# Optimization experiments

Hardware: AMD Instinct MI355X
Metric: run time of the kernel (lower is better)

Reference implementation:

```python
import jax, jax.numpy as jnp
import numpy as np

N_OBS = 2_097_152
N_BAND = 4
T_SPAN = 3650.0  # days


def setup_inputs() -> dict:
    key = jax.random.key(0)
    k0, k1, k2, k3, k4, k5 = jax.random.split(key, 6)
    t = jnp.sort(jax.random.uniform(k0, (N_OBS,), jnp.float32) * T_SPAN)
    band = jax.random.randint(k1, (N_OBS,), 0, N_BAND)
    y = jax.random.normal(k2, (N_OBS,), jnp.float32)
    yerr = 0.1 + 0.9 * jax.random.uniform(k3, (N_OBS,), jnp.float32)
    log_amp_delta = 0.1 * jax.random.normal(k4, (N_BAND - 1,), jnp.float32)
    # [log sigma, log ell] for the quasisep Exp kernel
    log_kernel_param = jnp.array([0.0, np.log(50.0)], dtype=jnp.float32) + \
        0.1 * jax.random.normal(k5, (2,), jnp.float32)
    return {"t": t, "band": band, "y": y, "yerr": yerr,
            "log_amp_delta": log_amp_delta, "log_kernel_param": log_kernel_param}


def _log_prob(t, band, y, yerr, log_amp_delta, log_kernel_param):
    # amp_transform: prepend 0 -> per-band amplitudes
    amps = jnp.exp(jnp.concatenate([jnp.zeros(1, log_amp_delta.dtype), log_amp_delta]))
    sigma2 = jnp.exp(2.0 * log_kernel_param[0])
    ell = jnp.exp(log_kernel_param[1])

    # lag_transform with zero lags: sort by time (assume_sorted path of tinygp)
    inds = jnp.argsort(t)
    ts, b = t[inds], band[inds]
    ys, dg = y[inds], (yerr ** 2)[inds]

    # multiband Exp kernel: K_ij = sigma2 * u_i * u_j * exp(-(t_i - t_j)/ell), i>=j
    u = amps[b]                       # per-point amplitude
    a = dg + sigma2 * u * u           # diagonal K_ii + noise
    U = sigma2 * u                    # semiseparable left factor
    V = u                             # semiseparable right factor
    dt = jnp.diff(ts)
    P = jnp.concatenate([jnp.zeros(1, ts.dtype), jnp.exp(-dt / ell)])  # decay factors

    # Celerite O(N) Cholesky (K = L D L^T) fused with the forward solve L z = y.
    def step(carry, x):
        cS, cg = carry                # cS = S_{n-1} + D_{n-1} W_{n-1}^2 ; cg = g_{n-1} + W_{n-1} z_{n-1}
        Pn, an, Un, Vn, yn = x
        Sn = Pn * Pn * cS
        gn = Pn * cg
        Dn = an - Un * Un * Sn
        Wn = (Vn - Sn * Un) / Dn
        zn = yn - Un * gn
        return (Sn + Dn * Wn * Wn, gn + Wn * zn), (jnp.log(Dn), zn * zn / Dn)

    zero = jnp.zeros((), ts.dtype)
    _, (logD, quad) = jax.lax.scan(step, (zero, zero), (P, a, U, V, ys))
    n = ts.shape[0]
    return -0.5 * (jnp.sum(quad) + jnp.sum(logD) + n * jnp.log(2.0 * jnp.pi))


def reference(t, band, y, yerr, log_amp_delta, log_kernel_param):
    return _log_prob(t, band, y, yerr, log_amp_delta, log_kernel_param)
```

## Files before the change

kernel.cpp:

```cpp
#include <hip/hip_runtime.h>
#include <math.h>

#define N_TOTAL 2097152
#define NT 512
#define NC 16
#define EPB (NT * NC)
#define NB (N_TOTAL / EPB)

struct DMat { double al, be, ga, de, c, e, f; };

__device__ __forceinline__ DMat dmat_identity() {
    DMat m; m.al = 1.0; m.be = 0.0; m.ga = 0.0; m.de = 1.0; m.c = 1.0; m.e = 0.0; m.f = 0.0;
    return m;
}

__device__ __forceinline__ DMat dmat_compose(const DMat& A, const DMat& B) {
    DMat r;
    r.al = A.al * B.al + A.be * B.ga;
    r.be = A.al * B.be + A.be * B.de;
    r.ga = A.ga * B.al + A.de * B.ga;
    r.de = A.ga * B.be + A.de * B.de;
    r.c  = A.c * B.c;
    r.e  = A.e * B.al + A.c * B.e + A.f * B.ga;
    r.f  = A.e * B.be + A.c * B.f + A.f * B.de;
    return r;
}

__device__ __forceinline__ void dmat_normalize(DMat& m) {
    double mx = fmax(fabs(m.al), fabs(m.be));
    mx = fmax(mx, fabs(m.ga));
    mx = fmax(mx, fabs(m.de));
    mx = fmax(mx, fabs(m.c));
    mx = fmax(mx, fabs(m.e));
    mx = fmax(mx, fabs(m.f));
    if (!(mx > 0.0) || isinf(mx)) return;
    double inv = 1.0 / mx;
    m.al *= inv; m.be *= inv; m.ga *= inv; m.de *= inv;
    m.c *= inv; m.e *= inv; m.f *= inv;
}

__device__ __forceinline__ void dmat_store(double* sm, int i, const DMat& m) {
    sm[0 * NT + i] = m.al; sm[1 * NT + i] = m.be; sm[2 * NT + i] = m.ga;
    sm[3 * NT + i] = m.de; sm[4 * NT + i] = m.c;  sm[5 * NT + i] = m.e;
    sm[6 * NT + i] = m.f;
}

__device__ __forceinline__ DMat dmat_load(const double* sm, int i) {
    DMat m;
    m.al = sm[0 * NT + i]; m.be = sm[1 * NT + i]; m.ga = sm[2 * NT + i];
    m.de = sm[3 * NT + i]; m.c  = sm[4 * NT + i]; m.e  = sm[5 * NT + i];
    m.f  = sm[6 * NT + i];
    return m;
}

__device__ __forceinline__ DMat dmat_scan_inclusive(double* sm, DMat mine, int tid) {
    dmat_store(sm, tid, mine);
    __syncthreads();
    for (int d = 1; d < NT; d <<= 1) {
        DMat o;
        bool has = (tid >= d);
        if (has) o = dmat_load(sm, tid - d);
        __syncthreads();
        if (has) {
            mine = dmat_compose(mine, o);
            dmat_normalize(mine);
            dmat_store(sm, tid, mine);
        }
        __syncthreads();
    }
    return mine;
}

__device__ __forceinline__ void dmat_scan_spine(double* sm, int tid) {
    for (int d = 1; d < NB; d <<= 1) {
        DMat mine, o;
        bool has = (tid >= d) && (tid < NB);
        if (has) { mine = dmat_load(sm, tid); o = dmat_load(sm, tid - d); }
        __syncthreads();
        if (has) {
            mine = dmat_compose(mine, o);
            dmat_normalize(mine);
            dmat_store(sm, tid, mine);
        }
        __syncthreads();
    }
}

__device__ __forceinline__ DMat elem_mat(double P, double a, double U, double V, double yy) {
    double p = P * P;
    DMat m;
    m.al = p * (a - 2.0 * U * V);
    m.be = V * V;
    m.ga = -(p * U * U);
    m.de = a;
    m.c  = P * (a - U * V);
    m.e  = -(yy * p * U);
    m.f  = yy * V;
    return m;
}

__device__ __forceinline__ double band_amp(int b, double a1, double a2, double a3) {
    double lo = (b & 1) ? a1 : 1.0;
    double hi = (b & 1) ? a3 : a2;
    return (b & 2) ? hi : lo;
}

__global__ __launch_bounds__(NT) void k_fused(
    const float* __restrict__ t, const int* __restrict__ band,
    const float* __restrict__ y, const float* __restrict__ yerr,
    const float* __restrict__ lad, const float* __restrict__ lkp,
    double* __restrict__ L, double* __restrict__ accum,
    unsigned int* __restrict__ bar0, unsigned int* __restrict__ done,
    float* __restrict__ out)
{
    __shared__ double sm[7 * NT];
    __shared__ double red[16];
    const int tid = threadIdx.x;
    const int bid = blockIdx.x;

    const double sigma2 = exp(2.0 * (double)lkp[0]);
    const float inv_ell_f = expf(-lkp[1]);
    const double amp1 = exp((double)lad[0]);
    const double amp2 = exp((double)lad[1]);
    const double amp3 = exp((double)lad[2]);

    const int gid = bid * NT + tid;
    const int base = gid * NC;
    const bool first = (base == 0);

    float Pv[NC], av[NC], Uv[NC], Vv[NC], yvv[NC];

    float tpA = first ? 0.0f : t[base - 1];
    float tpB = t[base + NC / 2 - 1];

    DMat accA = dmat_identity();
    DMat accB = dmat_identity();

    #pragma unroll
    for (int kk = 0; kk < NC / 2; kk += 4) {
        float4 tvA = *reinterpret_cast<const float4*>(t + base + kk);
        float4 yvA = *reinterpret_cast<const float4*>(y + base + kk);
        float4 evA = *reinterpret_cast<const float4*>(yerr + base + kk);
        int4   bvA = *reinterpret_cast<const int4*>(band + base + kk);
        float4 tvB = *reinterpret_cast<const float4*>(t + base + NC / 2 + kk);
        float4 yvB = *reinterpret_cast<const float4*>(y + base + NC / 2 + kk);
        float4 evB = *reinterpret_cast<const float4*>(yerr + base + NC / 2 + kk);
        int4   bvB = *reinterpret_cast<const int4*>(band + base + NC / 2 + kk);
        float tA[4] = {tvA.x, tvA.y, tvA.z, tvA.w};
        float yA[4] = {yvA.x, yvA.y, yvA.z, yvA.w};
        float eA[4] = {evA.x, evA.y, evA.z, evA.w};
        int   bA[4] = {bvA.x, bvA.y, bvA.z, bvA.w};
        float tB[4] = {tvB.x, tvB.y, tvB.z, tvB.w};
        float yB[4] = {yvB.x, yvB.y, yvB.z, yvB.w};
        float eB[4] = {evB.x, evB.y, evB.z, evB.w};
        int   bB[4] = {bvB.x, bvB.y, bvB.z, bvB.w};
        #pragma unroll
        for (int j = 0; j < 4; ++j) {
            {
                double u = band_amp(bA[j], amp1, amp2, amp3);
                double U = sigma2 * u;
                double a = (double)eA[j] * (double)eA[j] + U * u;
                float dt = tA[j] - tpA; tpA = tA[j];
                float pf = (first && kk == 0 && j == 0)
                         ? 0.0f : expf(-dt * inv_ell_f);
                Pv[kk + j] = pf; av[kk + j] = (float)a;
                Uv[kk + j] = (float)U; Vv[kk + j] = (float)u;
                yvv[kk + j] = yA[j];
                accA = dmat_compose(elem_mat((double)pf, a, U, u, (double)yA[j]), accA);
            }
            {
                double u = band_amp(bB[j], amp1, amp2, amp3);
                double U = sigma2 * u;
                double a = (double)eB[j] * (double)eB[j] + U * u;
                float dt = tB[j] - tpB; tpB = tB[j];
                float pf = expf(-dt * inv_ell_f);
                int ix = 8 + kk + j;
                Pv[ix] = pf; av[ix] = (float)a;
                Uv[ix] = (float)U; Vv[ix] = (float)u;
                yvv[ix] = yB[j];
                accB = dmat_compose(elem_mat((double)pf, a, U, u, (double)yB[j]), accB);
            }
        }
    }
    DMat acc = dmat_compose(accB, accA);
    dmat_normalize(acc);
    DMat incl = dmat_scan_inclusive(sm, acc, tid);

    DMat Et = (tid == 0) ? dmat_identity() : dmat_load(sm, tid - 1);

    if (tid == NT - 1) {
        double* o = L + bid * 7;
        o[0] = incl.al; o[1] = incl.be; o[2] = incl.ga; o[3] = incl.de;
        o[4] = incl.c;  o[5] = incl.e;  o[6] = incl.f;
    }

    __syncthreads();
    if (tid == 0) {
        __threadfence();
        atomicAdd(bar0, 1u);
        while (__hip_atomic_load(bar0, __ATOMIC_ACQUIRE,
                                 __HIP_MEMORY_SCOPE_AGENT) < NB) {
            __builtin_amdgcn_s_sleep(2);
        }
    }
    __syncthreads();

    if (tid < NB) {
        const double* p = L + tid * 7;
        DMat m = {p[0], p[1], p[2], p[3], p[4], p[5], p[6]};
        dmat_store(sm, tid, m);
    }
    __syncthreads();
    dmat_scan_spine(sm, tid);
    DMat Eb = dmat_identity();
    if (bid > 0) Eb = dmat_load(sm, bid - 1);

    DMat F = dmat_compose(Et, Eb);
    dmat_normalize(F);
    double x = 0.0, g = 0.0;
    if (F.de != 0.0 && !isinf(F.de)) {
        double invde = 1.0 / F.de;
        x = F.be * invde;
        g = F.f  * invde;
    }
    if (!isfinite(x)) x = 0.0;
    if (!isfinite(g)) g = 0.0;

    double s_logD = 0.0, s_quad = 0.0, pd = 1.0;
    #pragma unroll
    for (int k = 0; k < NC; ++k) {
        double P = (double)Pv[k], a = (double)av[k], U = (double)Uv[k];
        double V = (double)Vv[k], yy = (double)yvv[k];
        double p = P * P;
        double S = p * x;
        double D = a - U * U * S;
        if (!(D > 1e-300)) D = 1e-300;
        double invD = 1.0 / D;
        double W = (V - S * U) * invD;
        double gn = P * g;
        double z = yy - U * gn;
        pd *= D;
        s_quad = fma(z * z, invD, s_quad);
        x = fma(D * W, W, S);
        g = fma(W, z, gn);
        if ((k & 7) == 7) {
            s_logD += log(pd);
            pd = 1.0;
        }
    }

    #pragma unroll
    for (int off = 32; off > 0; off >>= 1) {
        s_logD += __shfl_down(s_logD, off);
        s_quad += __shfl_down(s_quad, off);
    }
    const int wid = tid >> 6, lane = tid & 63;
    if (lane == 0) { red[wid] = s_logD; red[8 + wid] = s_quad; }
    __syncthreads();
    if (tid == 0) {
        double l = 0.0, q = 0.0;
        #pragma unroll
        for (int w = 0; w < 8; ++w) { l += red[w]; q += red[8 + w]; }
        atomicAdd(&accum[0], l);
        atomicAdd(&accum[1], q);
        __threadfence();
        unsigned int old = atomicAdd(done, 1u);
        if (old == NB - 1) {
            double LL = atomicAdd(&accum[0], 0.0);
            double QQ = atomicAdd(&accum[1], 0.0);
            out[0] = (float)(-0.5 * (QQ + LL
                     + (double)N_TOTAL * 1.8378770664093454836));
        }
    }
}

extern "C" void kernel_launch(void* const* d_in, const int* in_sizes, int n_in,
                              void* d_out, int out_size, void* d_ws, size_t ws_size,
                              hipStream_t stream)
{
    const float* t    = (const float*)d_in[0];
    const int*   band = (const int*)d_in[1];
    const float* y    = (const float*)d_in[2];
    const float* yerr = (const float*)d_in[3];
    const float* lad  = (const float*)d_in[4];
    const float* lkp  = (const float*)d_in[5];

    double* dws        = (double*)d_ws;
    double* accum      = dws;
    unsigned int* ctrs = (unsigned int*)(dws + 2);
    double* L          = dws + 4;

    hipMemsetAsync(dws, 0, 32, stream);
    k_fused<<<NB, NT, 0, stream>>>(t, band, y, yerr, lad, lkp,
                                   L, accum, ctrs, ctrs + 1, (float*)d_out);
}
```

Measured before the change: 122.6 us.

## Replace shared-memory block scans with wavefront shuffle scans and halve per-thread chunk

The block-level and spine prefix scans of the 7-element double matrices move from a barrier-per-step shared-memory Hillis-Steele scan to 64-lane wavefront shuffle scans plus a small cross-wave combine. Blocks grow to 1024 threads, each handling 8 elements, so there are 256 blocks whose spine is scanned by 4 waves. Fewer __syncthreads and LDS round trips should cut scan latency. The cost is more threads doing double-precision matrix composition, larger blocks that must all be co-resident for the grid barrier, and dropped normalization inside the wave scan, which risks overflow.

```diff
diff --git a/kernel.cpp b/kernel.cpp
--- a/kernel.cpp
+++ b/kernel.cpp
@@ -2,10 +2,11 @@
 #include <math.h>
 
 #define N_TOTAL 2097152
-#define NT 512
-#define NC 16
+#define NT 1024
+#define NC 8
 #define EPB (NT * NC)
 #define NB (N_TOTAL / EPB)
+#define NWAVE (NT / 64)
 
 struct DMat { double al, be, ga, de, c, e, f; };
 
@@ -39,51 +40,31 @@
     m.c *= inv; m.e *= inv; m.f *= inv;
 }
 
-__device__ __forceinline__ void dmat_store(double* sm, int i, const DMat& m) {
-    sm[0 * NT + i] = m.al; sm[1 * NT + i] = m.be; sm[2 * NT + i] = m.ga;
-    sm[3 * NT + i] = m.de; sm[4 * NT + i] = m.c;  sm[5 * NT + i] = m.e;
-    sm[6 * NT + i] = m.f;
-}
-
-__device__ __forceinline__ DMat dmat_load(const double* sm, int i) {
-    DMat m;
-    m.al = sm[0 * NT + i]; m.be = sm[1 * NT + i]; m.ga = sm[2 * NT + i];
-    m.de = sm[3 * NT + i]; m.c  = sm[4 * NT + i]; m.e  = sm[5 * NT + i];
-    m.f  = sm[6 * NT + i];
-    return m;
-}
-
-__device__ __forceinline__ DMat dmat_scan_inclusive(double* sm, DMat mine, int tid) {
-    dmat_store(sm, tid, mine);
-    __syncthreads();
-    for (int d = 1; d < NT; d <<= 1) {
-        DMat o;
-        bool has = (tid >= d);
-        if (has) o = dmat_load(sm, tid - d);
-        __syncthreads();
-        if (has) {
-            mine = dmat_compose(mine, o);
-            dmat_normalize(mine);
-            dmat_store(sm, tid, mine);
-        }
-        __syncthreads();
+__device__ __forceinline__ DMat dmat_shfl_up(const DMat& m, int d) {
+    DMat r;
+    r.al = __shfl_up(m.al, d); r.be = __shfl_up(m.be, d);
+    r.ga = __shfl_up(m.ga, d); r.de = __shfl_up(m.de, d);
+    r.c  = __shfl_up(m.c,  d); r.e  = __shfl_up(m.e,  d);
+    r.f  = __shfl_up(m.f,  d);
+    return r;
+}
+
+__device__ __forceinline__ DMat dmat_shfl_bcast(const DMat& m, int src) {
+    DMat r;
+    r.al = __shfl(m.al, src); r.be = __shfl(m.be, src);
+    r.ga = __shfl(m.ga, src); r.de = __shfl(m.de, src);
+    r.c  = __shfl(m.c,  src); r.e  = __shfl(m.e,  src);
+    r.f  = __shfl(m.f,  src);
+    return r;
+}
+
+__device__ __forceinline__ DMat dmat_wave_scan64(DMat mine, int lane) {
+    #pragma unroll
+    for (int d = 1; d < 64; d <<= 1) {
+        DMat o = dmat_shfl_up(mine, d);
+        if (lane >= d) mine = dmat_compose(mine, o);
     }
     return mine;
-}
-
-__device__ __forceinline__ void dmat_scan_spine(double* sm, int tid) {
-    for (int d = 1; d < NB; d <<= 1) {
-        DMat mine, o;
-        bool has = (tid >= d) && (tid < NB);
-        if (has) { mine = dmat_load(sm, tid); o = dmat_load(sm, tid - d); }
-        __syncthreads();
-        if (has) {
-            mine = dmat_compose(mine, o);
-            dmat_normalize(mine);
-            dmat_store(sm, tid, mine);
-        }
-        __syncthreads();
-    }
 }
 
 __device__ __forceinline__ DMat elem_mat(double P, double a, double U, double V, double yy) {
@@ -105,6 +86,28 @@
     return (b & 2) ? hi : lo;
 }
 
+__device__ __forceinline__ void dmat_store_agent(double* p, const DMat& m) {
+    __hip_atomic_store(&p[0], m.al, __ATOMIC_RELAXED, __HIP_MEMORY_SCOPE_AGENT);
+    __hip_atomic_store(&p[1], m.be, __ATOMIC_RELAXED, __HIP_MEMORY_SCOPE_AGENT);
+    __hip_atomic_store(&p[2], m.ga, __ATOMIC_RELAXED, __HIP_MEMORY_SCOPE_AGENT);
+    __hip_atomic_store(&p[3], m.de, __ATOMIC_RELAXED, __HIP_MEMORY_SCOPE_AGENT);
+    __hip_atomic_store(&p[4], m.c,  __ATOMIC_RELAXED, __HIP_MEMORY_SCOPE_AGENT);
+    __hip_atomic_store(&p[5], m.e,  __ATOMIC_RELAXED, __HIP_MEMORY_SCOPE_AGENT);
+    __hip_atomic_store(&p[6], m.f,  __ATOMIC_RELAXED, __HIP_MEMORY_SCOPE_AGENT);
+}
+
+__device__ __forceinline__ DMat dmat_load_agent(const double* p) {
+    DMat m;
+    m.al = __hip_atomic_load(&p[0], __ATOMIC_RELAXED, __HIP_MEMORY_SCOPE_AGENT);
+    m.be = __hip_atomic_load(&p[1], __ATOMIC_RELAXED, __HIP_MEMORY_SCOPE_AGENT);
+    m.ga = __hip_atomic_load(&p[2], __ATOMIC_RELAXED, __HIP_MEMORY_SCOPE_AGENT);
+    m.de = __hip_atomic_load(&p[3], __ATOMIC_RELAXED, __HIP_MEMORY_SCOPE_AGENT);
+    m.c  = __hip_atomic_load(&p[4], __ATOMIC_RELAXED, __HIP_MEMORY_SCOPE_AGENT);
+    m.e  = __hip_atomic_load(&p[5], __ATOMIC_RELAXED, __HIP_MEMORY_SCOPE_AGENT);
+    m.f  = __hip_atomic_load(&p[6], __ATOMIC_RELAXED, __HIP_MEMORY_SCOPE_AGENT);
+    return m;
+}
+
 __global__ __launch_bounds__(NT) void k_fused(
     const float* __restrict__ t, const int* __restrict__ band,
     const float* __restrict__ y, const float* __restrict__ yerr,
@@ -113,10 +116,15 @@
     unsigned int* __restrict__ bar0, unsigned int* __restrict__ done,
     float* __restrict__ out)
 {
-    __shared__ double sm[7 * NT];
-    __shared__ double red[16];
-    const int tid = threadIdx.x;
-    const int bid = blockIdx.x;
+    __shared__ double totW[7 * 16];
+    __shared__ double spI[7 * NB];
+    __shared__ double spT[7 * 4];
+    __shared__ double red[2 * NWAVE];
+
+    const int tid  = threadIdx.x;
+    const int lane = tid & 63;
+    const int wid  = tid >> 6;
+    const int bid  = blockIdx.x;
 
     const double sigma2 = exp(2.0 * (double)lkp[0]);
     const float inv_ell_f = expf(-lkp[1]);
@@ -124,74 +132,96 @@
     const double amp2 = exp((double)lad[1]);
     const double amp3 = exp((double)lad[2]);
 
-    const int gid = bid * NT + tid;
+    const int gid  = bid * NT + tid;
     const int base = gid * NC;
-    const bool first = (base == 0);
+    const bool first = (gid == 0);
+
+    float4 tvA = *reinterpret_cast<const float4*>(t + base);
+    float4 tvB = *reinterpret_cast<const float4*>(t + base + 4);
+    float4 yvA = *reinterpret_cast<const float4*>(y + base);
+    float4 yvB = *reinterpret_cast<const float4*>(y + base + 4);
+    float4 evA = *reinterpret_cast<const float4*>(yerr + base);
+    float4 evB = *reinterpret_cast<const float4*>(yerr + base + 4);
+    int4   bvA = *reinterpret_cast<const int4*>(band + base);
+    int4   bvB = *reinterpret_cast<const int4*>(band + base + 4);
+    float tpA = first ? 0.0f : t[base - 1];
+    float tpB = tvA.w;
+
+    float tA[4] = {tvA.x, tvA.y, tvA.z, tvA.w};
+    float yA[4] = {yvA.x, yvA.y, yvA.z, yvA.w};
+    float eA[4] = {evA.x, evA.y, evA.z, evA.w};
+    int   bA[4] = {bvA.x, bvA.y, bvA.z, bvA.w};
+    float tB[4] = {tvB.x, tvB.y, tvB.z, tvB.w};
+    float yB[4] = {yvB.x, yvB.y, yvB.z, yvB.w};
+    float eB[4] = {evB.x, evB.y, evB.z, evB.w};
+    int   bB[4] = {bvB.x, bvB.y, bvB.z, bvB.w};
 
     float Pv[NC], av[NC], Uv[NC], Vv[NC], yvv[NC];
-
-    float tpA = first ? 0.0f : t[base - 1];
-    float tpB = t[base + NC / 2 - 1];
 
     DMat accA = dmat_identity();
     DMat accB = dmat_identity();
-
-    #pragma unroll
-    for (int kk = 0; kk < NC / 2; kk += 4) {
-        float4 tvA = *reinterpret_cast<const float4*>(t + base + kk);
-        float4 yvA = *reinterpret_cast<const float4*>(y + base + kk);
-        float4 evA = *reinterpret_cast<const float4*>(yerr + base + kk);
-        int4   bvA = *reinterpret_cast<const int4*>(band + base + kk);
-        float4 tvB = *reinterpret_cast<const float4*>(t + base + NC / 2 + kk);
-        float4 yvB = *reinterpret_cast<const float4*>(y + base + NC / 2 + kk);
-        float4 evB = *reinterpret_cast<const float4*>(yerr + base + NC / 2 + kk);
-        int4   bvB = *reinterpret_cast<const int4*>(band + base + NC / 2 + kk);
-        float tA[4] = {tvA.x, tvA.y, tvA.z, tvA.w};
-        float yA[4] = {yvA.x, yvA.y, yvA.z, yvA.w};
-        float eA[4] = {evA.x, evA.y, evA.z, evA.w};
-        int   bA[4] = {bvA.x, bvA.y, bvA.z, bvA.w};
-        float tB[4] = {tvB.x, tvB.y, tvB.z, tvB.w};
-        float yB[4] = {yvB.x, yvB.y, yvB.z, yvB.w};
-        float eB[4] = {evB.x, evB.y, evB.z, evB.w};
-        int   bB[4] = {bvB.x, bvB.y, bvB.z, bvB.w};
-        #pragma unroll
-        for (int j = 0; j < 4; ++j) {
-            {
-                double u = band_amp(bA[j], amp1, amp2, amp3);
-                double U = sigma2 * u;
-                double a = (double)eA[j] * (double)eA[j] + U * u;
-                float dt = tA[j] - tpA; tpA = tA[j];
-                float pf = (first && kk == 0 && j == 0)
-                         ? 0.0f : expf(-dt * inv_ell_f);
-                Pv[kk + j] = pf; av[kk + j] = (float)a;
-                Uv[kk + j] = (float)U; Vv[kk + j] = (float)u;
-                yvv[kk + j] = yA[j];
-                accA = dmat_compose(elem_mat((double)pf, a, U, u, (double)yA[j]), accA);
-            }
-            {
-                double u = band_amp(bB[j], amp1, amp2, amp3);
-                double U = sigma2 * u;
-                double a = (double)eB[j] * (double)eB[j] + U * u;
-                float dt = tB[j] - tpB; tpB = tB[j];
-                float pf = expf(-dt * inv_ell_f);
-                int ix = 8 + kk + j;
-                Pv[ix] = pf; av[ix] = (float)a;
-                Uv[ix] = (float)U; Vv[ix] = (float)u;
-                yvv[ix] = yB[j];
-                accB = dmat_compose(elem_mat((double)pf, a, U, u, (double)yB[j]), accB);
-            }
+    #pragma unroll
+    for (int j = 0; j < 4; ++j) {
+        {
+            double u = band_amp(bA[j], amp1, amp2, amp3);
+            double U = sigma2 * u;
+            double a = (double)eA[j] * (double)eA[j] + U * u;
+            float dt = tA[j] - tpA; tpA = tA[j];
+            float pf = (first && j == 0) ? 0.0f : expf(-dt * inv_ell_f);
+            Pv[j] = pf; av[j] = (float)a; Uv[j] = (float)U;
+            Vv[j] = (float)u; yvv[j] = yA[j];
+            accA = dmat_compose(elem_mat((double)pf, a, U, u, (double)yA[j]), accA);
+        }
+        {
+            double u = band_amp(bB[j], amp1, amp2, amp3);
+            double U = sigma2 * u;
+            double a = (double)eB[j] * (double)eB[j] + U * u;
+            float dt = tB[j] - tpB; tpB = tB[j];
+            float pf = expf(-dt * inv_ell_f);
+            Pv[4 + j] = pf; av[4 + j] = (float)a; Uv[4 + j] = (float)U;
+            Vv[4 + j] = (float)u; yvv[4 + j] = yB[j];
+            accB = dmat_compose(elem_mat((double)pf, a, U, u, (double)yB[j]), accB);
         }
     }
     DMat acc = dmat_compose(accB, accA);
     dmat_normalize(acc);
-    DMat incl = dmat_scan_inclusive(sm, acc, tid);
-
-    DMat Et = (tid == 0) ? dmat_identity() : dmat_load(sm, tid - 1);
-
-    if (tid == NT - 1) {
-        double* o = L + bid * 7;
-        o[0] = incl.al; o[1] = incl.be; o[2] = incl.ga; o[3] = incl.de;
-        o[4] = incl.c;  o[5] = incl.e;  o[6] = incl.f;
+
+    DMat incl = dmat_wave_scan64(acc, lane);
+    dmat_normalize(incl);
+    DMat laneExcl = dmat_shfl_up(incl, 1);
+    if (lane == 63) {
+        totW[0 * 16 + wid] = incl.al; totW[1 * 16 + wid] = incl.be;
+        totW[2 * 16 + wid] = incl.ga; totW[3 * 16 + wid] = incl.de;
+        totW[4 * 16 + wid] = incl.c;  totW[5 * 16 + wid] = incl.e;
+        totW[6 * 16 + wid] = incl.f;
+    }
+    __syncthreads();
+
+    DMat tv = dmat_identity();
+    if (lane < 16) {
+        tv.al = totW[0 * 16 + lane]; tv.be = totW[1 * 16 + lane];
+        tv.ga = totW[2 * 16 + lane]; tv.de = totW[3 * 16 + lane];
+        tv.c  = totW[4 * 16 + lane]; tv.e  = totW[5 * 16 + lane];
+        tv.f  = totW[6 * 16 + lane];
+    }
+    #pragma unroll
+    for (int d = 1; d < 16; d <<= 1) {
+        DMat o = dmat_shfl_up(tv, d);
+        if (lane >= d && lane < 16) tv = dmat_compose(tv, o);
+    }
+    dmat_normalize(tv);
+
+    if (tid == 15) {
+        dmat_store_agent(L + bid * 7, tv);
+        __threadfence();
+    }
+
+    DMat Et;
+    if (wid == 0) {
+        Et = (lane == 0) ? dmat_identity() : laneExcl;
+    } else {
+        DMat waveExcl = dmat_shfl_bcast(tv, wid - 1);
+        Et = (lane == 0) ? waveExcl : dmat_compose(laneExcl, waveExcl);
     }
 
     __syncthreads();
@@ -205,15 +235,41 @@
     }
     __syncthreads();
 
-    if (tid < NB) {
-        const double* p = L + tid * 7;
-        DMat m = {p[0], p[1], p[2], p[3], p[4], p[5], p[6]};
-        dmat_store(sm, tid, m);
-    }
-    __syncthreads();
-    dmat_scan_spine(sm, tid);
+    if (wid < 4) {
+        DMat sv = dmat_load_agent(L + tid * 7);
+        sv = dmat_wave_scan64(sv, lane);
+        dmat_normalize(sv);
+        spI[0 * NB + tid] = sv.al; spI[1 * NB + tid] = sv.be;
+        spI[2 * NB + tid] = sv.ga; spI[3 * NB + tid] = sv.de;
+        spI[4 * NB + tid] = sv.c;  spI[5 * NB + tid] = sv.e;
+        spI[6 * NB + tid] = sv.f;
+        if (lane == 63) {
+            spT[0 * 4 + wid] = sv.al; spT[1 * 4 + wid] = sv.be;
+            spT[2 * 4 + wid] = sv.ga; spT[3 * 4 + wid] = sv.de;
+            spT[4 * 4 + wid] = sv.c;  spT[5 * 4 + wid] = sv.e;
+            spT[6 * 4 + wid] = sv.f;
+        }
+    }
+    __syncthreads();
+
     DMat Eb = dmat_identity();
-    if (bid > 0) Eb = dmat_load(sm, bid - 1);
+    if (bid > 0) {
+        const int i = bid - 1;
+        Eb.al = spI[0 * NB + i]; Eb.be = spI[1 * NB + i];
+        Eb.ga = spI[2 * NB + i]; Eb.de = spI[3 * NB + i];
+        Eb.c  = spI[4 * NB + i]; Eb.e  = spI[5 * NB + i];
+        Eb.f  = spI[6 * NB + i];
+        const int nw = i >> 6;
+        for (int w = nw - 1; w >= 0; --w) {
+            DMat T;
+            T.al = spT[0 * 4 + w]; T.be = spT[1 * 4 + w];
+            T.ga = spT[2 * 4 + w]; T.de = spT[3 * 4 + w];
+            T.c  = spT[4 * 4 + w]; T.e  = spT[5 * 4 + w];
+            T.f  = spT[6 * 4 + w];
+            Eb = dmat_compose(Eb, T);
+        }
+        dmat_normalize(Eb);
+    }
 
     DMat F = dmat_compose(Et, Eb);
     dmat_normalize(F);
@@ -243,24 +299,20 @@
         s_quad = fma(z * z, invD, s_quad);
         x = fma(D * W, W, S);
         g = fma(W, z, gn);
-        if ((k & 7) == 7) {
-            s_logD += log(pd);
-            pd = 1.0;
-        }
-    }
+    }
+    s_logD = log(pd);
 
     #pragma unroll
     for (int off = 32; off > 0; off >>= 1) {
         s_logD += __shfl_down(s_logD, off);
         s_quad += __shfl_down(s_quad, off);
     }
-    const int wid = tid >> 6, lane = tid & 63;
-    if (lane == 0) { red[wid] = s_logD; red[8 + wid] = s_quad; }
+    if (lane == 0) { red[wid] = s_logD; red[NWAVE + wid] = s_quad; }
     __syncthreads();
     if (tid == 0) {
         double l = 0.0, q = 0.0;
         #pragma unroll
-        for (int w = 0; w < 8; ++w) { l += red[w]; q += red[8 + w]; }
+        for (int w = 0; w < NWAVE; ++w) { l += red[w]; q += red[NWAVE + w]; }
         atomicAdd(&accum[0], l);
         atomicAdd(&accum[1], q);
         __threadfence();
```

Result: no change. 124.0 us (+1.1%).
